# Kernel optimization log

Measured on AMD Instinct MI355X. Metric: run time of the kernel, lower is better.

## Reference

```python
import jax, jax.numpy as jnp
import numpy as np

# Model constants (from init_kwargs / _select_heads)
H = 8          # heads for dim=1024
KR = 16        # read/write top-k
CHUNK = 128    # chunk size for chunked memory update
ETA = 0.1      # update rate
FORGET = 0.01  # decay_lambda -> forget_base per chunk
LWIN = 512     # local_window = K (use_bypass=True)


def _l2norm(t, eps=1e-6):
    return t / (jnp.linalg.norm(t, axis=-1, keepdims=True) + eps)


def setup_inputs() -> dict:
    key = jax.random.key(0)
    ks = jax.random.split(key, 5)
    B, T, D, K = 2, 2048, 1024, 512
    x = jax.random.normal(ks[0], (B, T, D), dtype=jnp.float32)
    W_qkv = jax.random.normal(ks[1], (3 * D, D), dtype=jnp.float32) / np.sqrt(D)
    b_qkv = jnp.zeros((3 * D,), dtype=jnp.float32)
    W_o = jax.random.normal(ks[2], (D, D), dtype=jnp.float32) / np.sqrt(D)
    b_o = jnp.zeros((D,), dtype=jnp.float32)
    S_init = jax.random.normal(ks[3], (K, D), dtype=jnp.float32) / np.sqrt(D)
    read_temperature = jnp.ones((1,), dtype=jnp.float32)
    return {"x": x, "W_qkv": W_qkv, "b_qkv": b_qkv, "W_o": W_o,
            "b_o": b_o, "S_init": S_init, "read_temperature": read_temperature}


def reference(x, W_qkv, b_qkv, W_o, b_o, S_init, read_temperature):
    B, T, D = x.shape
    K = S_init.shape[0]
    dh = D // H
    scale = 1.0 / np.sqrt(dh)
    temp = read_temperature[0]

    # fused qkv projection, split to heads [B,H,T,dh]
    qkv = x @ W_qkv.T + b_qkv
    q, k, v = jnp.split(qkv, 3, axis=-1)
    to_h = lambda t: t.reshape(B, T, H, dh).transpose(0, 2, 1, 3)
    qh, kh, vh = to_h(q), to_h(k), to_h(v)

    # initial slot state from S_init: [K, D] -> [H, K, dh] -> [B,H,K,dh]
    slot = S_init.reshape(K, H, dh).transpose(1, 0, 2)
    slot_k0 = jnp.broadcast_to(_l2norm(slot), (B, H, K, dh))
    slot_v0 = jnp.broadcast_to(slot, (B, H, K, dh))

    nc = T // CHUNK
    # [nc, B, H, C, dh]
    to_c = lambda t: t.reshape(B, H, nc, CHUNK, dh).transpose(2, 0, 1, 3, 4)
    qc, kc, vc = to_c(qh), to_c(kh), to_c(vh)

    bi_g = jnp.arange(B)[:, None, None, None]   # gather indices
    hi_g = jnp.arange(H)[None, :, None, None]
    bi_s = jnp.arange(B)[:, None, None]         # scatter indices
    hi_s = jnp.arange(H)[None, :, None]

    def chunk_step(carry, inp):
        slot_k, slot_v = carry
        qt, kt, vt = inp  # [B,H,C,dh]
        # ---- top-k sparse read from slot memory ----
        rscores = jnp.einsum('bhcd,bhkd->bhck', qt, slot_k) * scale / temp
        rv, ri = jax.lax.top_k(rscores, KR)
        rp = jax.nn.softmax(rv, axis=-1)                 # [B,H,C,KR]
        sel_v = slot_v[bi_g, hi_g, ri]                   # [B,H,C,KR,dh]
        read = jnp.einsum('bhck,bhckd->bhcd', rp, sel_v)
        # ---- top-k write with orthogonal update + decay ----
        k_hat = _l2norm(kt)
        wscores = jnp.einsum('bhcd,bhkd->bhck', k_hat, slot_k)
        wv, wi = jax.lax.top_k(wscores, KR)
        wp = jax.nn.softmax(wv, axis=-1)
        sel_k = slot_k[bi_g, hi_g, wi]                   # [B,H,C,KR,dh]
        proj = jnp.einsum('bhcd,bhckd->bhck', vt, sel_k)
        v_orth = vt[:, :, :, None, :] - proj[..., None] * sel_k
        dv = ETA * wp[..., None] * v_orth                # [B,H,C,KR,dh]
        dk = ETA * wp[..., None] * (k_hat[:, :, :, None, :] - sel_k)
        idx = wi.reshape(B, H, CHUNK * KR)
        slot_v = (1.0 - FORGET) * slot_v
        slot_v = slot_v.at[bi_s, hi_s, idx].add(dv.reshape(B, H, CHUNK * KR, dh))
        slot_k = _l2norm(slot_k.at[bi_s, hi_s, idx].add(dk.reshape(B, H, CHUNK * KR, dh)))
        return (slot_k, slot_v), read

    _, reads = jax.lax.scan(chunk_step, (slot_k0, slot_v0), (qc, kc, vc))
    reads = reads.transpose(1, 2, 0, 3, 4).reshape(B, H, T, dh)

    # ---- local bypass: block-causal sliding-window attention (window=LWIN) ----
    nb = T // LWIN
    qb = qh.reshape(B, H, nb, LWIN, dh)
    kb = kh.reshape(B, H, nb, LWIN, dh)
    vb = vh.reshape(B, H, nb, LWIN, dh)
    zpad = jnp.zeros_like(kb[:, :, :1])
    kcat = jnp.concatenate([jnp.concatenate([zpad, kb[:, :, :-1]], axis=2), kb], axis=3)
    vcat = jnp.concatenate([jnp.concatenate([zpad, vb[:, :, :-1]], axis=2), vb], axis=3)
    s = jnp.einsum('bhnqd,bhnkd->bhnqk', qb, kcat) * scale  # [B,H,nb,LWIN,2*LWIN]
    i = jnp.arange(LWIN)[:, None]
    j = jnp.arange(2 * LWIN)[None, :]
    base = (j <= LWIN + i) & (j > i)                        # causal + window
    blk = (jnp.arange(nb) > 0)[:, None, None] | (j >= LWIN)[None]
    mask = base[None] & blk                                 # [nb,LWIN,2*LWIN]
    s = jnp.where(mask[None, None], s, -1e30)
    a = jax.nn.softmax(s, axis=-1)
    local = jnp.einsum('bhnqk,bhnkd->bhnqd', a, vcat).reshape(B, H, T, dh)

    y = (reads + local).transpose(0, 2, 1, 3).reshape(B, T, D)
    return y @ W_o.T + b_o
```

## Files before the change

### kernel.cpp

```cpp
#include <hip/hip_runtime.h>

typedef unsigned short u16;
typedef unsigned int u32;
typedef unsigned long long u64;
typedef __attribute__((ext_vector_type(8))) short bf16x8;
typedef __attribute__((ext_vector_type(4))) float f32x4;

#define B2 2
#define T2 2048
#define D2 1024
#define H2 8
#define DH 128
#define KSL 512
#define CH 128
#define NCH 16
#define NBH 16
#define MAGIC 0x13579BDFu

__device__ __forceinline__ float bf2f(u32 h) { union { u32 u; float f; } x; x.u = h << 16; return x.f; }
__device__ __forceinline__ u16 f2bf(float f) {
  union { float f; u32 u; } x; x.f = f;
  return (u16)((x.u + 0x7FFFu + ((x.u >> 16) & 1u)) >> 16);
}
__device__ __forceinline__ u32 pack2(float a, float b) { return (u32)f2bf(a) | ((u32)f2bf(b) << 16); }

__device__ __forceinline__ u32 cload32(const void* p) {
  return __hip_atomic_load((u32*)p, __ATOMIC_RELAXED, __HIP_MEMORY_SCOPE_AGENT);
}
__device__ __forceinline__ void cstore32(void* p, u32 v) {
  __hip_atomic_store((u32*)p, v, __ATOMIC_RELAXED, __HIP_MEMORY_SCOPE_AGENT);
}
__device__ __forceinline__ u64 cload64(const void* p) {
  return __hip_atomic_load((u64*)p, __ATOMIC_RELAXED, __HIP_MEMORY_SCOPE_AGENT);
}
__device__ __forceinline__ void cstore64(void* p, u64 v) {
  __hip_atomic_store((u64*)p, v, __ATOMIC_RELAXED, __HIP_MEMORY_SCOPE_AGENT);
}
__device__ __forceinline__ float2 cloadf2(const float* p) {
  union { u64 q; float2 f; } x; x.q = cload64(p); return x.f;
}
__device__ __forceinline__ void cstoref2(float* p, float2 v) {
  union { float2 f; u64 q; } x; x.f = v; cstore64(p, x.q);
}

__global__ __launch_bounds__(256) void qkv_gemm(
    const float* __restrict__ x, const float* __restrict__ w,
    const float* __restrict__ bias, u16* __restrict__ qhb,
    u16* __restrict__ khb, u16* __restrict__ vhb) {
  __shared__ u16 As[128 * 72];
  __shared__ u16 Bs[128 * 72];
  const int tid = threadIdx.x;
  const int lane = tid & 63, wv = tid >> 6;
  const int quad = lane >> 4, l15 = lane & 15;
  const int m0 = blockIdx.y * 128, n0 = blockIdx.x * 128;
  const int wr = wv >> 1, wc = wv & 1;
  f32x4 acc[4][4];
#pragma unroll
  for (int i = 0; i < 4; ++i)
#pragma unroll
    for (int j = 0; j < 4; ++j) acc[i][j] = f32x4{0.f, 0.f, 0.f, 0.f};
  const int f4c = tid & 15, r0 = tid >> 4;
  for (int kt = 0; kt < 16; ++kt) {
#pragma unroll
    for (int i = 0; i < 8; ++i) {
      int row = r0 + i * 16;
      float4 a = *(const float4*)(x + (size_t)(m0 + row) * 1024 + kt * 64 + f4c * 4);
      float4 b = *(const float4*)(w + (size_t)(n0 + row) * 1024 + kt * 64 + f4c * 4);
      *(uint2*)(&As[row * 72 + f4c * 4]) = make_uint2(pack2(a.x, a.y), pack2(a.z, a.w));
      *(uint2*)(&Bs[row * 72 + f4c * 4]) = make_uint2(pack2(b.x, b.y), pack2(b.z, b.w));
    }
    __syncthreads();
#pragma unroll
    for (int ks = 0; ks < 2; ++ks) {
      bf16x8 af[4], bff[4];
#pragma unroll
      for (int rt = 0; rt < 4; ++rt)
        af[rt] = *(const bf16x8*)(&As[(wr * 64 + rt * 16 + l15) * 72 + ks * 32 + quad * 8]);
#pragma unroll
      for (int ct = 0; ct < 4; ++ct)
        bff[ct] = *(const bf16x8*)(&Bs[(wc * 64 + ct * 16 + l15) * 72 + ks * 32 + quad * 8]);
#pragma unroll
      for (int rt = 0; rt < 4; ++rt)
#pragma unroll
        for (int ct = 0; ct < 4; ++ct)
          acc[rt][ct] = __builtin_amdgcn_mfma_f32_16x16x32_bf16(af[rt], bff[ct], acc[rt][ct], 0, 0, 0);
    }
    __syncthreads();
  }
#pragma unroll
  for (int ct = 0; ct < 4; ++ct) {
    int n = n0 + wc * 64 + ct * 16 + l15;
    float bv = bias[n];
    int sec = n >> 10, rr2 = n & 1023, hh = rr2 >> 7, dd = rr2 & 127;
    u16* dst = (sec == 0) ? qhb : (sec == 1) ? khb : vhb;
#pragma unroll
    for (int rt = 0; rt < 4; ++rt)
#pragma unroll
      for (int rg = 0; rg < 4; ++rg) {
        int m = m0 + wr * 64 + rt * 16 + quad * 4 + rg;
        int bb = m >> 11, tt = m & 2047;
        dst[((size_t)(bb * 8 + hh) * T2 + tt) * DH + dd] = f2bf(acc[rt][ct][rg] + bv);
      }
  }
}

__global__ __launch_bounds__(256) void attn_kernel(
    const u16* __restrict__ qhb, const u16* __restrict__ khb,
    const u16* __restrict__ vhb, float* __restrict__ yin) {
  __shared__ u16 Pls[128 * 72];
  __shared__ u16 VT[128 * 72];
  const int tid = threadIdx.x;
  const int lane = tid & 63, wv = tid >> 6;
  const int quad = lane >> 4, l15 = lane & 15;
  const int bh = blockIdx.y, qt = blockIdx.x;
  const int t0 = qt * 128;
  const int b = bh >> 3, h = bh & 7;
  f32x4 Oa[2][8];
  float mrow[2][4], lrow[2][4];
#pragma unroll
  for (int rt = 0; rt < 2; ++rt) {
#pragma unroll
    for (int dt = 0; dt < 8; ++dt) Oa[rt][dt] = f32x4{0.f, 0.f, 0.f, 0.f};
#pragma unroll
    for (int rg = 0; rg < 4; ++rg) { mrow[rt][rg] = -1e30f; lrow[rt][rg] = 0.f; }
  }
  const u16* qbase = qhb + ((size_t)bh * T2 + t0) * DH;
  int j0 = t0 / 64 - 8; if (j0 < 0) j0 = 0;
  int j1 = t0 / 64 + 1;
  for (int jt = j0; jt <= j1; ++jt) {
    int kv0 = jt * 64;
    __syncthreads();
    {
      int r = tid & 63, dq = tid >> 6;
      const u16* vrow = vhb + ((size_t)bh * T2 + kv0 + r) * DH + dq * 32;
#pragma unroll
      for (int u = 0; u < 4; ++u) {
        uint4 pv = *(const uint4*)(vrow + u * 8);
        int d0 = dq * 32 + u * 8;
        VT[(d0 + 0) * 72 + r] = (u16)(pv.x); VT[(d0 + 1) * 72 + r] = (u16)(pv.x >> 16);
        VT[(d0 + 2) * 72 + r] = (u16)(pv.y); VT[(d0 + 3) * 72 + r] = (u16)(pv.y >> 16);
        VT[(d0 + 4) * 72 + r] = (u16)(pv.z); VT[(d0 + 5) * 72 + r] = (u16)(pv.z >> 16);
        VT[(d0 + 6) * 72 + r] = (u16)(pv.w); VT[(d0 + 7) * 72 + r] = (u16)(pv.w >> 16);
      }
    }
    f32x4 Sa[2][4];
#pragma unroll
    for (int rt = 0; rt < 2; ++rt)
#pragma unroll
      for (int ct = 0; ct < 4; ++ct) Sa[rt][ct] = f32x4{0.f, 0.f, 0.f, 0.f};
#pragma unroll
    for (int ks = 0; ks < 4; ++ks) {
      bf16x8 a0 = *(const bf16x8*)(qbase + (size_t)(wv * 32 + l15) * DH + ks * 32 + quad * 8);
      bf16x8 a1 = *(const bf16x8*)(qbase + (size_t)(wv * 32 + 16 + l15) * DH + ks * 32 + quad * 8);
#pragma unroll
      for (int ct = 0; ct < 4; ++ct) {
        bf16x8 bb = *(const bf16x8*)(khb + ((size_t)bh * T2 + kv0 + ct * 16 + l15) * DH + ks * 32 + quad * 8);
        Sa[0][ct] = __builtin_amdgcn_mfma_f32_16x16x32_bf16(a0, bb, Sa[0][ct], 0, 0, 0);
        Sa[1][ct] = __builtin_amdgcn_mfma_f32_16x16x32_bf16(a1, bb, Sa[1][ct], 0, 0, 0);
      }
    }
#pragma unroll
    for (int rt = 0; rt < 2; ++rt)
#pragma unroll
      for (int rg = 0; rg < 4; ++rg) {
        int row = wv * 32 + rt * 16 + quad * 4 + rg;
        int qp = t0 + row;
        float vals[4];
        float mx = -1e30f;
#pragma unroll
        for (int ct = 0; ct < 4; ++ct) {
          int kp = kv0 + ct * 16 + l15;
          float s = Sa[rt][ct][rg] * 0.08838834764831845f;
          bool ok = (kp <= qp) && (kp + 512 > qp);
          s = ok ? s : -1e30f;
          vals[ct] = s;
          mx = fmaxf(mx, s);
        }
#pragma unroll
        for (int sh = 1; sh < 16; sh <<= 1) mx = fmaxf(mx, __shfl_xor(mx, sh));
        float mold = mrow[rt][rg];
        float mnew = fmaxf(mold, mx);
        float alpha = __expf(mold - mnew);
        float rsum = 0.f;
        float pv_[4];
#pragma unroll
        for (int ct = 0; ct < 4; ++ct) {
          float p = (vals[ct] < -1e29f) ? 0.f : __expf(vals[ct] - mnew);
          pv_[ct] = p; rsum += p;
        }
#pragma unroll
        for (int sh = 1; sh < 16; sh <<= 1) rsum += __shfl_xor(rsum, sh);
        lrow[rt][rg] = lrow[rt][rg] * alpha + rsum;
        mrow[rt][rg] = mnew;
#pragma unroll
        for (int dt = 0; dt < 8; ++dt) Oa[rt][dt][rg] *= alpha;
#pragma unroll
        for (int ct = 0; ct < 4; ++ct) Pls[row * 72 + ct * 16 + l15] = f2bf(pv_[ct]);
      }
    __syncthreads();
#pragma unroll
    for (int ks = 0; ks < 2; ++ks) {
      bf16x8 a0 = *(const bf16x8*)(&Pls[(wv * 32 + l15) * 72 + ks * 32 + quad * 8]);
      bf16x8 a1 = *(const bf16x8*)(&Pls[(wv * 32 + 16 + l15) * 72 + ks * 32 + quad * 8]);
#pragma unroll
      for (int dt = 0; dt < 8; ++dt) {
        bf16x8 bb = *(const bf16x8*)(&VT[(dt * 16 + l15) * 72 + ks * 32 + quad * 8]);
        Oa[0][dt] = __builtin_amdgcn_mfma_f32_16x16x32_bf16(a0, bb, Oa[0][dt], 0, 0, 0);
        Oa[1][dt] = __builtin_amdgcn_mfma_f32_16x16x32_bf16(a1, bb, Oa[1][dt], 0, 0, 0);
      }
    }
  }
#pragma unroll
  for (int rt = 0; rt < 2; ++rt)
#pragma unroll
    for (int rg = 0; rg < 4; ++rg) {
      int row = wv * 32 + rt * 16 + quad * 4 + rg;
      float invl = 1.0f / lrow[rt][rg];
#pragma unroll
      for (int dt = 0; dt < 8; ++dt)
        yin[((size_t)b * T2 + t0 + row) * D2 + h * DH + dt * 16 + l15] = Oa[rt][dt][rg] * invl;
    }
}

struct ScanArgs {
  const u16* qhb; const u16* khb; const u16* vhb;
  float* yin; float* sk; float* sv; u16* skb; u16* khatb;
  u32* cnt; uint4* entries;
  u32* barcnt; u32* bargen; u32* ready;
  const float* sinit; const float* temp;
};

__device__ __forceinline__ void bh_barrier(u32* cnt, u32* gen) {
  asm volatile("" ::: "memory");
  __syncthreads();
  if (threadIdx.x == 0) {
    u32 g = cload32(gen);
    u32 a = __hip_atomic_fetch_add(cnt, 1u, __ATOMIC_RELAXED, __HIP_MEMORY_SCOPE_AGENT);
    if ((a & 15u) == 15u) {
      cstore32(gen, g + 1u);
    } else {
      while (cload32(gen) == g) __builtin_amdgcn_s_sleep(2);
    }
    __builtin_amdgcn_fence(__ATOMIC_ACQUIRE, "agent");
  }
  __syncthreads();
  asm volatile("" ::: "memory");
}

__device__ __forceinline__ void topk16(const float* rowp, int lane, volatile u64* candw,
                                       float& p_out, u32& idx_out) {
  u32 mono[8];
#pragma unroll
  for (int j = 0; j < 8; ++j) {
    float f = rowp[j * 64 + lane];
    u32 u = __float_as_uint(f);
    mono[j] = ((int)u < 0) ? ~u : (u | 0x80000000u);
  }
  u32 mx = mono[0];
#pragma unroll
  for (int j = 1; j < 8; ++j) mx = max(mx, mono[j]);
  u32 s = mx;
#pragma unroll
  for (int k = 2; k <= 64; k <<= 1) {
#pragma unroll
    for (int j = k >> 1; j > 0; j >>= 1) {
      u32 o = (u32)__shfl_xor((int)s, j);
      bool keep_min = (((lane & k) == 0) == ((lane & j) == 0));
      u32 mn = min(s, o), mxx = max(s, o);
      s = keep_min ? mn : mxx;
    }
  }
  u32 thr = (u32)__shfl((int)s, 48);
  u32 base = 0;
#pragma unroll
  for (int j = 0; j < 8; ++j) {
    bool pred = (mono[j] >= thr);
    u64 mask = __ballot(pred);
    u32 pos = base + (u32)__popcll(mask & ((1ull << lane) - 1ull));
    if (pred && pos < 64u)
      candw[pos] = (((u64)mono[j]) << 32) | (u64)(0xFFFFFFFFu - (u32)(j * 64 + lane));
    base += (u32)__popcll(mask);
  }
  __threadfence_block();
  u32 cntc = base < 64u ? base : 64u;
  u64 key = ((u32)lane < cntc) ? candw[lane] : 0ull;
#pragma unroll
  for (int k = 2; k <= 64; k <<= 1) {
#pragma unroll
    for (int j = k >> 1; j > 0; j >>= 1) {
      u64 o = __shfl_xor(key, j);
      bool keep_min = (((lane & k) == 0) == ((lane & j) == 0));
      u64 mn = key < o ? key : o;
      u64 mxx = key < o ? o : key;
      key = keep_min ? mn : mxx;
    }
  }
  u32 um = (u32)(key >> 32);
  float val = __uint_as_float((um & 0x80000000u) ? (um & 0x7FFFFFFFu) : ~um);
  idx_out = 0xFFFFFFFFu - (u32)(key & 0xFFFFFFFFull);
  float mtop = __shfl(val, 63);
  float e = __expf(val - mtop);
  float ssum = e;
#pragma unroll
  for (int sh = 1; sh < 16; sh <<= 1) ssum += __shfl_xor(ssum, sh);
  p_out = e / ssum;
}

__global__ __launch_bounds__(512, 2) void scan_kernel(ScanArgs A) {
  const int tid = threadIdx.x;
  const int lane = tid & 63, wv = tid >> 6;
  const int quad = lane >> 4, l15 = lane & 15;
  const int xcd = blockIdx.x & 7;
  const int wi = blockIdx.x >> 3;
  const int bh = xcd * 2 + (wi >> 4);
  const int blk = wi & 15;
  const int b = bh >> 3, h = bh & 7;
  __shared__ u16 khat_ls[8 * 136];
  __shared__ float scores_r[8 * 520];
  __shared__ float scores_w[8 * 520];
  __shared__ u64 cand[8][64];

  const float invtemp = 1.0f / A.temp[0];
  const float sc_r = 0.08838834764831845f * invtemp;

#pragma unroll 1
  for (int i = 0; i < 4; ++i) {
    int s = blk * 32 + wv * 4 + i;
    float2 v2 = *(const float2*)(A.sinit + (size_t)s * 1024 + h * 128 + lane * 2);
    float ssq = v2.x * v2.x + v2.y * v2.y;
#pragma unroll
    for (int sh = 1; sh < 64; sh <<= 1) ssq += __shfl_xor(ssq, sh);
    float inv = 1.0f / (sqrtf(ssq) + 1e-6f);
    size_t off = ((size_t)bh * KSL + s) * DH + lane * 2;
    cstoref2(A.sk + off, make_float2(v2.x * inv, v2.y * inv));
    cstoref2(A.sv + off, v2);
    cstore32(A.skb + off, pack2(v2.x * inv, v2.y * inv));
    if (lane == 0) cstore32(&A.cnt[bh * KSL + s], 0u);
  }
  if (blk == 0 && tid == 0) { cstore32(A.barcnt + bh, 0u); cstore32(A.bargen + bh, 0u); }
  __syncthreads();
  if (tid == 0) {
    cstore32(&A.ready[bh * 16 + blk], MAGIC);
    for (int i = 0; i < 16; ++i)
      while (cload32(&A.ready[bh * 16 + i]) != MAGIC) __builtin_amdgcn_s_sleep(2);
    __builtin_amdgcn_fence(__ATOMIC_ACQUIRE, "agent");
  }
  __syncthreads();

  u32* bcnt = A.barcnt + bh;
  u32* bgen = A.bargen + bh;

#pragma unroll 1
  for (int ci = 0; ci < NCH; ++ci) {
    const int t0base = ci * CH;
    const int c = blk * 8 + wv;
    const int trow = t0base + c;
    {
      u32 kraw = *(const u32*)(A.khb + ((size_t)bh * T2 + trow) * DH + lane * 2);
      float k0 = bf2f(kraw & 0xFFFFu), k1 = bf2f(kraw >> 16);
      float ssq = k0 * k0 + k1 * k1;
#pragma unroll
      for (int sh = 1; sh < 64; sh <<= 1) ssq += __shfl_xor(ssq, sh);
      float inv = 1.0f / (sqrtf(ssq) + 1e-6f);
      u32 pk = pack2(k0 * inv, k1 * inv);
      *(u32*)(&khat_ls[wv * 136 + lane * 2]) = pk;
      cstore32(A.khatb + ((size_t)bh * CH + c) * DH + lane * 2, pk);
    }
    __syncthreads();
    {
      const u16* qbase = A.qhb + ((size_t)bh * T2 + t0base + blk * 8) * DH;
      const u16* sbase = A.skb + (size_t)bh * KSL * DH;
      f32x4 acc[4];
#pragma unroll
      for (int ct = 0; ct < 4; ++ct) acc[ct] = f32x4{0.f, 0.f, 0.f, 0.f};
#pragma unroll
      for (int ks = 0; ks < 4; ++ks) {
        bf16x8 a;
        if (l15 < 8)
          a = *(const bf16x8*)(qbase + (size_t)l15 * DH + ks * 32 + quad * 8);
        else
          a = *(const bf16x8*)(&khat_ls[(l15 - 8) * 136 + ks * 32 + quad * 8]);
#pragma unroll
        for (int ct = 0; ct < 4; ++ct) {
          bf16x8 bb = *(const bf16x8*)(sbase + (size_t)(wv * 64 + ct * 16 + l15) * DH + ks * 32 + quad * 8);
          acc[ct] = __builtin_amdgcn_mfma_f32_16x16x32_bf16(a, bb, acc[ct], 0, 0, 0);
        }
      }
#pragma unroll
      for (int ct = 0; ct < 4; ++ct)
#pragma unroll
        for (int rg = 0; rg < 4; ++rg) {
          int m = quad * 4 + rg;
          int col = wv * 64 + ct * 16 + l15;
          if (m < 8) scores_r[m * 520 + col] = acc[ct][rg] * sc_r;
          else       scores_w[(m - 8) * 520 + col] = acc[ct][rg];
        }
    }
    __syncthreads();
    {
      float p; u32 sidx;
      topk16(&scores_r[wv * 520], lane, cand[wv], p, sidx);
      float acc0 = 0.f, acc1 = 0.f;
      const float* svb = A.sv + (size_t)bh * KSL * DH;
#pragma unroll
      for (int r = 0; r < 16; ++r) {
        float pr = __shfl(p, 63 - r);
        u32 ir = (u32)__shfl((int)sidx, 63 - r);
        float2 vv = *(const float2*)(svb + (size_t)ir * DH + lane * 2);
        acc0 += pr * vv.x; acc1 += pr * vv.y;
      }
      {
        float* yp = A.yin + ((size_t)b * T2 + trow) * D2 + h * DH + lane * 2;
        float2 y0 = cloadf2(yp);
        cstoref2(yp, make_float2(y0.x + acc0, y0.y + acc1));
      }

      float wp; u32 widx;
      topk16(&scores_w[wv * 520], lane, cand[wv], wp, widx);
      const int r = lane >> 2, g = lane & 3;
      float wr = __shfl(wp, 63 - r);
      u32 ir = (u32)__shfl((int)widx, 63 - r);
      const float* kb = A.sk + ((size_t)bh * KSL + ir) * DH + g * 32;
      const u16* vb = A.vhb + ((size_t)bh * T2 + trow) * DH + g * 32;
      float part = 0.f;
#pragma unroll
      for (int u2 = 0; u2 < 4; ++u2) {
        uint4 vvp = *(const uint4*)(vb + u2 * 8);
        float4 k0 = *(const float4*)(kb + u2 * 8);
        float4 k1 = *(const float4*)(kb + u2 * 8 + 4);
        part += bf2f(vvp.x & 0xFFFFu) * k0.x + bf2f(vvp.x >> 16) * k0.y
              + bf2f(vvp.y & 0xFFFFu) * k0.z + bf2f(vvp.y >> 16) * k0.w
              + bf2f(vvp.z & 0xFFFFu) * k1.x + bf2f(vvp.z >> 16) * k1.y
              + bf2f(vvp.w & 0xFFFFu) * k1.z + bf2f(vvp.w >> 16) * k1.w;
      }
      part += __shfl_xor(part, 1);
      part += __shfl_xor(part, 2);
      if (g == 0) {
        u32 pos = __hip_atomic_fetch_add(&A.cnt[bh * KSL + ir], 1u,
                                         __ATOMIC_RELAXED, __HIP_MEMORY_SCOPE_AGENT);
        if (pos < 128u) {
          u32* e = (u32*)(A.entries + ((size_t)bh * KSL + ir) * 128 + pos);
          cstore64(e, (u64)(u32)c | ((u64)__float_as_uint(wr) << 32));
          cstore32(e + 2, __float_as_uint(part));
        }
      }
    }
    bh_barrier(bcnt, bgen);
#pragma unroll 1
    for (int i = 0; i < 4; ++i) {
      int s = blk * 32 + wv * 4 + i;
      size_t slotoff = (size_t)bh * KSL + s;
      size_t roff = slotoff * DH + lane * 2;
      u32 n = cload32(&A.cnt[slotoff]);
      const uint4* ebase = A.entries + slotoff * 128;
      uint4 ep[4];
#pragma unroll
      for (int j = 0; j < 4; ++j) ep[j] = ebase[j];
      float2 V = *(const float2*)(A.sv + roff);
      float2 Kr = *(const float2*)(A.sk + roff);
      float dv0 = 0, dv1 = 0, dk0 = 0, dk1 = 0;
      u32 nd = n < 128u ? n : 128u;
      u32 mf = nd < 4u ? nd : 4u;
      {
        u32 vr[4], hr[4];
#pragma unroll
        for (int j = 0; j < 4; ++j) if (j < (int)mf) {
          u32 c2 = ep[j].x;
          vr[j] = *(const u32*)(A.vhb + ((size_t)bh * T2 + t0base + c2) * DH + lane * 2);
          hr[j] = *(const u32*)(A.khatb + ((size_t)bh * CH + c2) * DH + lane * 2);
        }
#pragma unroll
        for (int j = 0; j < 4; ++j) if (j < (int)mf) {
          float wpe = __uint_as_float(ep[j].y), pj = __uint_as_float(ep[j].z);
          dv0 += wpe * (bf2f(vr[j] & 0xFFFFu) - pj * Kr.x);
          dv1 += wpe * (bf2f(vr[j] >> 16) - pj * Kr.y);
          dk0 += wpe * (bf2f(hr[j] & 0xFFFFu) - Kr.x);
          dk1 += wpe * (bf2f(hr[j] >> 16) - Kr.y);
        }
      }
#pragma unroll 1
      for (u32 base2 = 4; base2 < nd; base2 += 8) {
        u32 m = nd - base2; if (m > 8u) m = 8u;
        uint4 eb[8];
#pragma unroll
        for (int j = 0; j < 8; ++j) if (j < (int)m) eb[j] = ebase[base2 + j];
        u32 vr[8], hr[8];
#pragma unroll
        for (int j = 0; j < 8; ++j) if (j < (int)m) {
          u32 c2 = eb[j].x;
          vr[j] = *(const u32*)(A.vhb + ((size_t)bh * T2 + t0base + c2) * DH + lane * 2);
          hr[j] = *(const u32*)(A.khatb + ((size_t)bh * CH + c2) * DH + lane * 2);
        }
#pragma unroll
        for (int j = 0; j < 8; ++j) if (j < (int)m) {
          float wpe = __uint_as_float(eb[j].y), pj = __uint_as_float(eb[j].z);
          dv0 += wpe * (bf2f(vr[j] & 0xFFFFu) - pj * Kr.x);
          dv1 += wpe * (bf2f(vr[j] >> 16) - pj * Kr.y);
          dk0 += wpe * (bf2f(hr[j] & 0xFFFFu) - Kr.x);
          dk1 += wpe * (bf2f(hr[j] >> 16) - Kr.y);
        }
      }
      cstoref2(A.sv + roff, make_float2(0.99f * V.x + 0.1f * dv0, 0.99f * V.y + 0.1f * dv1));
      if (n > 0u) {
        float u0 = Kr.x + 0.1f * dk0, u1 = Kr.y + 0.1f * dk1;
        float ssq = u0 * u0 + u1 * u1;
#pragma unroll
        for (int sh = 1; sh < 64; sh <<= 1) ssq += __shfl_xor(ssq, sh);
        float inv = 1.0f / (sqrtf(ssq) + 1e-6f);
        u0 *= inv; u1 *= inv;
        cstoref2(A.sk + roff, make_float2(u0, u1));
        cstore32(A.skb + roff, pack2(u0, u1));
      }
      if (lane == 0) cstore32(&A.cnt[slotoff], 0u);
    }
    bh_barrier(bcnt, bgen);
  }
}

__global__ __launch_bounds__(256) void out_gemm(
    const float* __restrict__ yin, const float* __restrict__ w,
    const float* __restrict__ bias, float* __restrict__ out) {
  __shared__ u16 As[128 * 72];
  __shared__ u16 Bs[128 * 72];
  const int tid = threadIdx.x;
  const int lane = tid & 63, wv = tid >> 6;
  const int quad = lane >> 4, l15 = lane & 15;
  const int m0 = blockIdx.y * 128, n0 = blockIdx.x * 128;
  const int wr = wv >> 1, wc = wv & 1;
  f32x4 acc[4][4];
#pragma unroll
  for (int i = 0; i < 4; ++i)
#pragma unroll
    for (int j = 0; j < 4; ++j) acc[i][j] = f32x4{0.f, 0.f, 0.f, 0.f};
  const int f4c = tid & 15, r0 = tid >> 4;
  for (int kt = 0; kt < 16; ++kt) {
#pragma unroll
    for (int i = 0; i < 8; ++i) {
      int row = r0 + i * 16;
      float4 a = *(const float4*)(yin + (size_t)(m0 + row) * 1024 + kt * 64 + f4c * 4);
      float4 b = *(const float4*)(w + (size_t)(n0 + row) * 1024 + kt * 64 + f4c * 4);
      *(uint2*)(&As[row * 72 + f4c * 4]) = make_uint2(pack2(a.x, a.y), pack2(a.z, a.w));
      *(uint2*)(&Bs[row * 72 + f4c * 4]) = make_uint2(pack2(b.x, b.y), pack2(b.z, b.w));
    }
    __syncthreads();
#pragma unroll
    for (int ks = 0; ks < 2; ++ks) {
      bf16x8 af[4], bff[4];
#pragma unroll
      for (int rt = 0; rt < 4; ++rt)
        af[rt] = *(const bf16x8*)(&As[(wr * 64 + rt * 16 + l15) * 72 + ks * 32 + quad * 8]);
#pragma unroll
      for (int ct = 0; ct < 4; ++ct)
        bff[ct] = *(const bf16x8*)(&Bs[(wc * 64 + ct * 16 + l15) * 72 + ks * 32 + quad * 8]);
#pragma unroll
      for (int rt = 0; rt < 4; ++rt)
#pragma unroll
        for (int ct = 0; ct < 4; ++ct)
          acc[rt][ct] = __builtin_amdgcn_mfma_f32_16x16x32_bf16(af[rt], bff[ct], acc[rt][ct], 0, 0, 0);
    }
    __syncthreads();
  }
#pragma unroll
  for (int ct = 0; ct < 4; ++ct) {
    int n = n0 + wc * 64 + ct * 16 + l15;
    float bv = bias[n];
#pragma unroll
    for (int rt = 0; rt < 4; ++rt)
#pragma unroll
      for (int rg = 0; rg < 4; ++rg) {
        int m = m0 + wr * 64 + rt * 16 + quad * 4 + rg;
        out[(size_t)m * 1024 + n] = acc[rt][ct][rg] + bv;
      }
  }
}

extern "C" void kernel_launch(void* const* d_in, const int* in_sizes, int n_in,
                              void* d_out, int out_size, void* d_ws, size_t ws_size,
                              hipStream_t stream) {
  const float* x = (const float*)d_in[0];
  const float* Wqkv = (const float*)d_in[1];
  const float* bqkv = (const float*)d_in[2];
  const float* Wo = (const float*)d_in[3];
  const float* bo = (const float*)d_in[4];
  const float* Sinit = (const float*)d_in[5];
  const float* temp = (const float*)d_in[6];
  float* out = (float*)d_out;

  char* p = (char*)d_ws;
  auto take = [&](size_t bytes) { char* r = p; p += (bytes + 255) & ~(size_t)255; return r; };
  u16* qhb = (u16*)take((size_t)NBH * T2 * DH * 2);
  u16* khb = (u16*)take((size_t)NBH * T2 * DH * 2);
  u16* vhb = (u16*)take((size_t)NBH * T2 * DH * 2);
  float* yin = (float*)take((size_t)B2 * T2 * D2 * 4);
  float* sk = (float*)take((size_t)NBH * KSL * DH * 4);
  float* sv = (float*)take((size_t)NBH * KSL * DH * 4);
  u16* skb = (u16*)take((size_t)NBH * KSL * DH * 2);
  u16* khatb = (u16*)take((size_t)NBH * CH * DH * 2);
  u32* cnt = (u32*)take((size_t)NBH * KSL * 4);
  uint4* entries = (uint4*)take((size_t)NBH * KSL * 128 * 16);
  u32* barcnt = (u32*)take(64 * 4);
  u32* bargen = (u32*)take(64 * 4);
  u32* ready = (u32*)take(NBH * 16 * 4);

  hipLaunchKernelGGL(qkv_gemm, dim3(24, 32), dim3(256), 0, stream, x, Wqkv, bqkv, qhb, khb, vhb);
  hipLaunchKernelGGL(attn_kernel, dim3(16, 16), dim3(256), 0, stream, qhb, khb, vhb, yin);
  ScanArgs sa{qhb, khb, vhb, yin, sk, sv, skb, khatb, cnt, entries, barcnt, bargen, ready, Sinit, temp};
  hipLaunchKernelGGL(scan_kernel, dim3(256), dim3(512), 0, stream, sa);
  hipLaunchKernelGGL(out_gemm, dim3(8, 32), dim3(256), 0, stream, yin, Wo, bo, out);
}
```

Baseline: 837.2 us.

## Restructure scan: precompute normalized keys, register-resident slots, dual top-k, lighter barriers

Key normalization moves out of the per-chunk loop into a prologue that overwrites khb in place. This removes the khat staging buffer and one __syncthreads per chunk. Slot K/V rows owned by each wave are kept in registers across chunks instead of being reloaded from global memory. The read and write top-k selections are interleaved in one dual routine so their shuffle chains can overlap. The first barrier of each chunk skips its acquire fence. The cost is more register pressure and a reliance on the relaxed barrier still being correct. The in-place khb overwrite also assumes attn_kernel has finished with the unnormalized keys.

Measured after the change: 906.9 us. +8.3%, slower.

```diff
diff --git a/kernel.cpp b/kernel.cpp
--- a/kernel.cpp
+++ b/kernel.cpp
@@ -223,14 +223,14 @@
 }
 
 struct ScanArgs {
-  const u16* qhb; const u16* khb; const u16* vhb;
-  float* yin; float* sk; float* sv; u16* skb; u16* khatb;
+  const u16* qhb; u16* khb; const u16* vhb;
+  float* yin; float* sk; float* sv; u16* skb;
   u32* cnt; uint4* entries;
   u32* barcnt; u32* bargen; u32* ready;
   const float* sinit; const float* temp;
 };
 
-__device__ __forceinline__ void bh_barrier(u32* cnt, u32* gen) {
+__device__ __forceinline__ void bh_barrier(u32* cnt, u32* gen, bool do_inv) {
   asm volatile("" ::: "memory");
   __syncthreads();
   if (threadIdx.x == 0) {
@@ -241,69 +241,100 @@
     } else {
       while (cload32(gen) == g) __builtin_amdgcn_s_sleep(2);
     }
-    __builtin_amdgcn_fence(__ATOMIC_ACQUIRE, "agent");
+    if (do_inv)
+      __builtin_amdgcn_fence(__ATOMIC_ACQUIRE, "agent");
   }
   __syncthreads();
   asm volatile("" ::: "memory");
 }
 
-__device__ __forceinline__ void topk16(const float* rowp, int lane, volatile u64* candw,
-                                       float& p_out, u32& idx_out) {
-  u32 mono[8];
+__device__ __forceinline__ void topk16_dual(
+    const float* rp0, const float* rp1, int lane,
+    volatile u64* cw0, volatile u64* cw1,
+    float& p0_out, u32& i0_out, float& p1_out, u32& i1_out) {
+  u32 mono[2][8];
 #pragma unroll
   for (int j = 0; j < 8; ++j) {
-    float f = rowp[j * 64 + lane];
-    u32 u = __float_as_uint(f);
-    mono[j] = ((int)u < 0) ? ~u : (u | 0x80000000u);
-  }
-  u32 mx = mono[0];
-#pragma unroll
-  for (int j = 1; j < 8; ++j) mx = max(mx, mono[j]);
-  u32 s = mx;
+    u32 u0 = __float_as_uint(rp0[j * 64 + lane]);
+    u32 u1 = __float_as_uint(rp1[j * 64 + lane]);
+    mono[0][j] = ((int)u0 < 0) ? ~u0 : (u0 | 0x80000000u);
+    mono[1][j] = ((int)u1 < 0) ? ~u1 : (u1 | 0x80000000u);
+  }
+  u32 sv_[2];
+#pragma unroll
+  for (int s = 0; s < 2; ++s) {
+    u32 mx = mono[s][0];
+#pragma unroll
+    for (int j = 1; j < 8; ++j) mx = max(mx, mono[s][j]);
+    sv_[s] = mx;
+  }
 #pragma unroll
   for (int k = 2; k <= 64; k <<= 1) {
 #pragma unroll
     for (int j = k >> 1; j > 0; j >>= 1) {
-      u32 o = (u32)__shfl_xor((int)s, j);
-      bool keep_min = (((lane & k) == 0) == ((lane & j) == 0));
-      u32 mn = min(s, o), mxx = max(s, o);
-      s = keep_min ? mn : mxx;
-    }
-  }
-  u32 thr = (u32)__shfl((int)s, 48);
-  u32 base = 0;
+      bool km = (((lane & k) == 0) == ((lane & j) == 0));
+#pragma unroll
+      for (int s = 0; s < 2; ++s) {
+        u32 o = (u32)__shfl_xor((int)sv_[s], j);
+        u32 mn = min(sv_[s], o), mxx = max(sv_[s], o);
+        sv_[s] = km ? mn : mxx;
+      }
+    }
+  }
+  u32 thr[2] = { (u32)__shfl((int)sv_[0], 48), (u32)__shfl((int)sv_[1], 48) };
+  u32 base[2] = { 0u, 0u };
 #pragma unroll
   for (int j = 0; j < 8; ++j) {
-    bool pred = (mono[j] >= thr);
-    u64 mask = __ballot(pred);
-    u32 pos = base + (u32)__popcll(mask & ((1ull << lane) - 1ull));
-    if (pred && pos < 64u)
-      candw[pos] = (((u64)mono[j]) << 32) | (u64)(0xFFFFFFFFu - (u32)(j * 64 + lane));
-    base += (u32)__popcll(mask);
+#pragma unroll
+    for (int s = 0; s < 2; ++s) {
+      bool pred = (mono[s][j] >= thr[s]);
+      u64 mask = __ballot(pred);
+      u32 pos = base[s] + (u32)__popcll(mask & ((1ull << lane) - 1ull));
+      volatile u64* cw = s ? cw1 : cw0;
+      if (pred && pos < 64u)
+        cw[pos] = (((u64)mono[s][j]) << 32) | (u64)(0xFFFFFFFFu - (u32)(j * 64 + lane));
+      base[s] += (u32)__popcll(mask);
+    }
   }
   __threadfence_block();
-  u32 cntc = base < 64u ? base : 64u;
-  u64 key = ((u32)lane < cntc) ? candw[lane] : 0ull;
+  u64 key[2];
+  {
+    u32 c0 = base[0] < 64u ? base[0] : 64u;
+    u32 c1 = base[1] < 64u ? base[1] : 64u;
+    key[0] = ((u32)lane < c0) ? cw0[lane] : 0ull;
+    key[1] = ((u32)lane < c1) ? cw1[lane] : 0ull;
+  }
 #pragma unroll
   for (int k = 2; k <= 64; k <<= 1) {
 #pragma unroll
     for (int j = k >> 1; j > 0; j >>= 1) {
-      u64 o = __shfl_xor(key, j);
-      bool keep_min = (((lane & k) == 0) == ((lane & j) == 0));
-      u64 mn = key < o ? key : o;
-      u64 mxx = key < o ? o : key;
-      key = keep_min ? mn : mxx;
-    }
-  }
-  u32 um = (u32)(key >> 32);
-  float val = __uint_as_float((um & 0x80000000u) ? (um & 0x7FFFFFFFu) : ~um);
-  idx_out = 0xFFFFFFFFu - (u32)(key & 0xFFFFFFFFull);
-  float mtop = __shfl(val, 63);
-  float e = __expf(val - mtop);
-  float ssum = e;
-#pragma unroll
-  for (int sh = 1; sh < 16; sh <<= 1) ssum += __shfl_xor(ssum, sh);
-  p_out = e / ssum;
+      bool km = (((lane & k) == 0) == ((lane & j) == 0));
+#pragma unroll
+      for (int s = 0; s < 2; ++s) {
+        u64 o = __shfl_xor(key[s], j);
+        u64 mn = key[s] < o ? key[s] : o;
+        u64 mxx = key[s] < o ? o : key[s];
+        key[s] = km ? mn : mxx;
+      }
+    }
+  }
+  float e[2], ssum[2]; u32 idx[2];
+#pragma unroll
+  for (int s = 0; s < 2; ++s) {
+    u32 um = (u32)(key[s] >> 32);
+    float val = __uint_as_float((um & 0x80000000u) ? (um & 0x7FFFFFFFu) : ~um);
+    idx[s] = 0xFFFFFFFFu - (u32)(key[s] & 0xFFFFFFFFull);
+    float mtop = __shfl(val, 63);
+    e[s] = __expf(val - mtop);
+    ssum[s] = e[s];
+  }
+#pragma unroll
+  for (int sh = 1; sh < 16; sh <<= 1) {
+    ssum[0] += __shfl_xor(ssum[0], sh);
+    ssum[1] += __shfl_xor(ssum[1], sh);
+  }
+  p0_out = e[0] / ssum[0]; i0_out = idx[0];
+  p1_out = e[1] / ssum[1]; i1_out = idx[1];
 }
 
 __global__ __launch_bounds__(512, 2) void scan_kernel(ScanArgs A) {
@@ -315,14 +346,15 @@
   const int bh = xcd * 2 + (wi >> 4);
   const int blk = wi & 15;
   const int b = bh >> 3, h = bh & 7;
-  __shared__ u16 khat_ls[8 * 136];
   __shared__ float scores_r[8 * 520];
   __shared__ float scores_w[8 * 520];
-  __shared__ u64 cand[8][64];
+  __shared__ u64 cand0[8][64];
+  __shared__ u64 cand1[8][64];
 
   const float invtemp = 1.0f / A.temp[0];
   const float sc_r = 0.08838834764831845f * invtemp;
 
+  float2 Vreg[4], Kreg[4];
 #pragma unroll 1
   for (int i = 0; i < 4; ++i) {
     int s = blk * 32 + wv * 4 + i;
@@ -331,11 +363,24 @@
 #pragma unroll
     for (int sh = 1; sh < 64; sh <<= 1) ssq += __shfl_xor(ssq, sh);
     float inv = 1.0f / (sqrtf(ssq) + 1e-6f);
+    Vreg[i] = v2;
+    Kreg[i] = make_float2(v2.x * inv, v2.y * inv);
     size_t off = ((size_t)bh * KSL + s) * DH + lane * 2;
-    cstoref2(A.sk + off, make_float2(v2.x * inv, v2.y * inv));
+    cstoref2(A.sk + off, Kreg[i]);
     cstoref2(A.sv + off, v2);
-    cstore32(A.skb + off, pack2(v2.x * inv, v2.y * inv));
+    cstore32(A.skb + off, pack2(Kreg[i].x, Kreg[i].y));
     if (lane == 0) cstore32(&A.cnt[bh * KSL + s], 0u);
+  }
+#pragma unroll 1
+  for (int ci = 0; ci < NCH; ++ci) {
+    int trow = ci * CH + blk * 8 + wv;
+    u32 kraw = *(const u32*)(A.khb + ((size_t)bh * T2 + trow) * DH + lane * 2);
+    float k0 = bf2f(kraw & 0xFFFFu), k1 = bf2f(kraw >> 16);
+    float ssq = k0 * k0 + k1 * k1;
+#pragma unroll
+    for (int sh = 1; sh < 64; sh <<= 1) ssq += __shfl_xor(ssq, sh);
+    float inv = 1.0f / (sqrtf(ssq) + 1e-6f);
+    cstore32(A.khb + ((size_t)bh * T2 + trow) * DH + lane * 2, pack2(k0 * inv, k1 * inv));
   }
   if (blk == 0 && tid == 0) { cstore32(A.barcnt + bh, 0u); cstore32(A.bargen + bh, 0u); }
   __syncthreads();
@@ -349,26 +394,15 @@
 
   u32* bcnt = A.barcnt + bh;
   u32* bgen = A.bargen + bh;
+  const int c = blk * 8 + wv;
 
 #pragma unroll 1
   for (int ci = 0; ci < NCH; ++ci) {
     const int t0base = ci * CH;
-    const int c = blk * 8 + wv;
     const int trow = t0base + c;
     {
-      u32 kraw = *(const u32*)(A.khb + ((size_t)bh * T2 + trow) * DH + lane * 2);
-      float k0 = bf2f(kraw & 0xFFFFu), k1 = bf2f(kraw >> 16);
-      float ssq = k0 * k0 + k1 * k1;
-#pragma unroll
-      for (int sh = 1; sh < 64; sh <<= 1) ssq += __shfl_xor(ssq, sh);
-      float inv = 1.0f / (sqrtf(ssq) + 1e-6f);
-      u32 pk = pack2(k0 * inv, k1 * inv);
-      *(u32*)(&khat_ls[wv * 136 + lane * 2]) = pk;
-      cstore32(A.khatb + ((size_t)bh * CH + c) * DH + lane * 2, pk);
-    }
-    __syncthreads();
-    {
       const u16* qbase = A.qhb + ((size_t)bh * T2 + t0base + blk * 8) * DH;
+      const u16* hbase = A.khb + ((size_t)bh * T2 + t0base + blk * 8) * DH;
       const u16* sbase = A.skb + (size_t)bh * KSL * DH;
       f32x4 acc[4];
 #pragma unroll
@@ -379,7 +413,7 @@
         if (l15 < 8)
           a = *(const bf16x8*)(qbase + (size_t)l15 * DH + ks * 32 + quad * 8);
         else
-          a = *(const bf16x8*)(&khat_ls[(l15 - 8) * 136 + ks * 32 + quad * 8]);
+          a = *(const bf16x8*)(hbase + (size_t)(l15 - 8) * DH + ks * 32 + quad * 8);
 #pragma unroll
         for (int ct = 0; ct < 4; ++ct) {
           bf16x8 bb = *(const bf16x8*)(sbase + (size_t)(wv * 64 + ct * 16 + l15) * DH + ks * 32 + quad * 8);
@@ -398,8 +432,9 @@
     }
     __syncthreads();
     {
-      float p; u32 sidx;
-      topk16(&scores_r[wv * 520], lane, cand[wv], p, sidx);
+      float p, wp; u32 sidx, widx;
+      topk16_dual(&scores_r[wv * 520], &scores_w[wv * 520], lane,
+                  cand0[wv], cand1[wv], p, sidx, wp, widx);
       float acc0 = 0.f, acc1 = 0.f;
       const float* svb = A.sv + (size_t)bh * KSL * DH;
 #pragma unroll
@@ -414,9 +449,6 @@
         float2 y0 = cloadf2(yp);
         cstoref2(yp, make_float2(y0.x + acc0, y0.y + acc1));
       }
-
-      float wp; u32 widx;
-      topk16(&scores_w[wv * 520], lane, cand[wv], wp, widx);
       const int r = lane >> 2, g = lane & 3;
       float wr = __shfl(wp, 63 - r);
       u32 ir = (u32)__shfl((int)widx, 63 - r);
@@ -445,75 +477,92 @@
         }
       }
     }
-    bh_barrier(bcnt, bgen);
+    bh_barrier(bcnt, bgen, false);
+    {
+      u32 n4[4]; u64 e0[4][4]; u32 e1[4][4];
+      size_t soff[4];
+#pragma unroll
+      for (int i = 0; i < 4; ++i) {
+        soff[i] = (size_t)bh * KSL + blk * 32 + wv * 4 + i;
+        n4[i] = cload32(&A.cnt[soff[i]]);
+        const u32* eb = (const u32*)(A.entries + soff[i] * 128);
+#pragma unroll
+        for (int j = 0; j < 4; ++j) {
+          e0[i][j] = cload64(eb + j * 4);
+          e1[i][j] = cload32(eb + j * 4 + 2);
+        }
+      }
+      u32 vr[4][4], hr[4][4];
+#pragma unroll
+      for (int i = 0; i < 4; ++i) {
+        u32 nd = n4[i] < 128u ? n4[i] : 128u;
+        u32 mfi = nd < 4u ? nd : 4u;
+#pragma unroll
+        for (int j = 0; j < 4; ++j) if (j < (int)mfi) {
+          u32 c2 = (u32)e0[i][j];
+          vr[i][j] = *(const u32*)(A.vhb + ((size_t)bh * T2 + t0base + c2) * DH + lane * 2);
+          hr[i][j] = *(const u32*)(A.khb + ((size_t)bh * T2 + t0base + c2) * DH + lane * 2);
+        }
+      }
+#pragma unroll
+      for (int i = 0; i < 4; ++i) {
+        u32 nd = n4[i] < 128u ? n4[i] : 128u;
+        u32 mfi = nd < 4u ? nd : 4u;
+        float dv0 = 0, dv1 = 0, dk0 = 0, dk1 = 0;
+#pragma unroll
+        for (int j = 0; j < 4; ++j) if (j < (int)mfi) {
+          float wpe = __uint_as_float((u32)(e0[i][j] >> 32)), pj = __uint_as_float(e1[i][j]);
+          dv0 += wpe * (bf2f(vr[i][j] & 0xFFFFu) - pj * Kreg[i].x);
+          dv1 += wpe * (bf2f(vr[i][j] >> 16) - pj * Kreg[i].y);
+          dk0 += wpe * (bf2f(hr[i][j] & 0xFFFFu) - Kreg[i].x);
+          dk1 += wpe * (bf2f(hr[i][j] >> 16) - Kreg[i].y);
+        }
+        if (nd > 4u) {
+          const u32* ebase = (const u32*)(A.entries + soff[i] * 128);
 #pragma unroll 1
-    for (int i = 0; i < 4; ++i) {
-      int s = blk * 32 + wv * 4 + i;
-      size_t slotoff = (size_t)bh * KSL + s;
-      size_t roff = slotoff * DH + lane * 2;
-      u32 n = cload32(&A.cnt[slotoff]);
-      const uint4* ebase = A.entries + slotoff * 128;
-      uint4 ep[4];
-#pragma unroll
-      for (int j = 0; j < 4; ++j) ep[j] = ebase[j];
-      float2 V = *(const float2*)(A.sv + roff);
-      float2 Kr = *(const float2*)(A.sk + roff);
-      float dv0 = 0, dv1 = 0, dk0 = 0, dk1 = 0;
-      u32 nd = n < 128u ? n : 128u;
-      u32 mf = nd < 4u ? nd : 4u;
-      {
-        u32 vr[4], hr[4];
-#pragma unroll
-        for (int j = 0; j < 4; ++j) if (j < (int)mf) {
-          u32 c2 = ep[j].x;
-          vr[j] = *(const u32*)(A.vhb + ((size_t)bh * T2 + t0base + c2) * DH + lane * 2);
-          hr[j] = *(const u32*)(A.khatb + ((size_t)bh * CH + c2) * DH + lane * 2);
-        }
-#pragma unroll
-        for (int j = 0; j < 4; ++j) if (j < (int)mf) {
-          float wpe = __uint_as_float(ep[j].y), pj = __uint_as_float(ep[j].z);
-          dv0 += wpe * (bf2f(vr[j] & 0xFFFFu) - pj * Kr.x);
-          dv1 += wpe * (bf2f(vr[j] >> 16) - pj * Kr.y);
-          dk0 += wpe * (bf2f(hr[j] & 0xFFFFu) - Kr.x);
-          dk1 += wpe * (bf2f(hr[j] >> 16) - Kr.y);
-        }
-      }
-#pragma unroll 1
-      for (u32 base2 = 4; base2 < nd; base2 += 8) {
-        u32 m = nd - base2; if (m > 8u) m = 8u;
-        uint4 eb[8];
-#pragma unroll
-        for (int j = 0; j < 8; ++j) if (j < (int)m) eb[j] = ebase[base2 + j];
-        u32 vr[8], hr[8];
-#pragma unroll
-        for (int j = 0; j < 8; ++j) if (j < (int)m) {
-          u32 c2 = eb[j].x;
-          vr[j] = *(const u32*)(A.vhb + ((size_t)bh * T2 + t0base + c2) * DH + lane * 2);
-          hr[j] = *(const u32*)(A.khatb + ((size_t)bh * CH + c2) * DH + lane * 2);
-        }
-#pragma unroll
-        for (int j = 0; j < 8; ++j) if (j < (int)m) {
-          float wpe = __uint_as_float(eb[j].y), pj = __uint_as_float(eb[j].z);
-          dv0 += wpe * (bf2f(vr[j] & 0xFFFFu) - pj * Kr.x);
-          dv1 += wpe * (bf2f(vr[j] >> 16) - pj * Kr.y);
-          dk0 += wpe * (bf2f(hr[j] & 0xFFFFu) - Kr.x);
-          dk1 += wpe * (bf2f(hr[j] >> 16) - Kr.y);
-        }
-      }
-      cstoref2(A.sv + roff, make_float2(0.99f * V.x + 0.1f * dv0, 0.99f * V.y + 0.1f * dv1));
-      if (n > 0u) {
-        float u0 = Kr.x + 0.1f * dk0, u1 = Kr.y + 0.1f * dk1;
-        float ssq = u0 * u0 + u1 * u1;
-#pragma unroll
-        for (int sh = 1; sh < 64; sh <<= 1) ssq += __shfl_xor(ssq, sh);
-        float inv = 1.0f / (sqrtf(ssq) + 1e-6f);
-        u0 *= inv; u1 *= inv;
-        cstoref2(A.sk + roff, make_float2(u0, u1));
-        cstore32(A.skb + roff, pack2(u0, u1));
-      }
-      if (lane == 0) cstore32(&A.cnt[slotoff], 0u);
-    }
-    bh_barrier(bcnt, bgen);
+          for (u32 b2 = 4; b2 < nd; b2 += 8) {
+            u32 m = nd - b2; if (m > 8u) m = 8u;
+            u64 f0[8]; u32 f1[8];
+#pragma unroll
+            for (int j = 0; j < 8; ++j) if (j < (int)m) {
+              const u32* ep = ebase + (size_t)(b2 + j) * 4;
+              f0[j] = cload64(ep);
+              f1[j] = cload32(ep + 2);
+            }
+            u32 wr2[8], hr2[8];
+#pragma unroll
+            for (int j = 0; j < 8; ++j) if (j < (int)m) {
+              u32 c2 = (u32)f0[j];
+              wr2[j] = *(const u32*)(A.vhb + ((size_t)bh * T2 + t0base + c2) * DH + lane * 2);
+              hr2[j] = *(const u32*)(A.khb + ((size_t)bh * T2 + t0base + c2) * DH + lane * 2);
+            }
+#pragma unroll
+            for (int j = 0; j < 8; ++j) if (j < (int)m) {
+              float wpe = __uint_as_float((u32)(f0[j] >> 32)), pj = __uint_as_float(f1[j]);
+              dv0 += wpe * (bf2f(wr2[j] & 0xFFFFu) - pj * Kreg[i].x);
+              dv1 += wpe * (bf2f(wr2[j] >> 16) - pj * Kreg[i].y);
+              dk0 += wpe * (bf2f(hr2[j] & 0xFFFFu) - Kreg[i].x);
+              dk1 += wpe * (bf2f(hr2[j] >> 16) - Kreg[i].y);
+            }
+          }
+        }
+        Vreg[i] = make_float2(0.99f * Vreg[i].x + 0.1f * dv0, 0.99f * Vreg[i].y + 0.1f * dv1);
+        size_t roff = soff[i] * DH + lane * 2;
+        cstoref2(A.sv + roff, Vreg[i]);
+        if (n4[i] > 0u) {
+          float u0 = Kreg[i].x + 0.1f * dk0, u1 = Kreg[i].y + 0.1f * dk1;
+          float ssq = u0 * u0 + u1 * u1;
+#pragma unroll
+          for (int sh = 1; sh < 64; sh <<= 1) ssq += __shfl_xor(ssq, sh);
+          float inv = 1.0f / (sqrtf(ssq) + 1e-6f);
+          Kreg[i] = make_float2(u0 * inv, u1 * inv);
+          cstoref2(A.sk + roff, Kreg[i]);
+          cstore32(A.skb + roff, pack2(Kreg[i].x, Kreg[i].y));
+        }
+        if (lane == 0) cstore32(&A.cnt[soff[i]], 0u);
+      }
+    }
+    bh_barrier(bcnt, bgen, true);
   }
 }
 
@@ -595,7 +644,6 @@
   float* sk = (float*)take((size_t)NBH * KSL * DH * 4);
   float* sv = (float*)take((size_t)NBH * KSL * DH * 4);
   u16* skb = (u16*)take((size_t)NBH * KSL * DH * 2);
-  u16* khatb = (u16*)take((size_t)NBH * CH * DH * 2);
   u32* cnt = (u32*)take((size_t)NBH * KSL * 4);
   uint4* entries = (uint4*)take((size_t)NBH * KSL * 128 * 16);
   u32* barcnt = (u32*)take(64 * 4);
@@ -604,7 +652,7 @@
 
   hipLaunchKernelGGL(qkv_gemm, dim3(24, 32), dim3(256), 0, stream, x, Wqkv, bqkv, qhb, khb, vhb);
   hipLaunchKernelGGL(attn_kernel, dim3(16, 16), dim3(256), 0, stream, qhb, khb, vhb, yin);
-  ScanArgs sa{qhb, khb, vhb, yin, sk, sv, skb, khatb, cnt, entries, barcnt, bargen, ready, Sinit, temp};
+  ScanArgs sa{qhb, khb, vhb, yin, sk, sv, skb, cnt, entries, barcnt, bargen, ready, Sinit, temp};
   hipLaunchKernelGGL(scan_kernel, dim3(256), dim3(512), 0, stream, sa);
   hipLaunchKernelGGL(out_gemm, dim3(8, 32), dim3(256), 0, stream, yin, Wo, bo, out);
 }
```
